# Optimization experiments

Hardware: AMD Instinct MI355X
Metric: run time of the kernel (lower is better)

The kernel has to match this reference:

```python
import jax, jax.numpy as jnp
import numpy as np

B, Z, H, W, C = 8, 16, 32, 32, 512
C8 = C // 8
N = Z * H * W
EPS = 1e-3  # Keras BatchNormalization default epsilon


def setup_inputs() -> dict:
    key = jax.random.key(0)
    ks = jax.random.split(key, 8)
    scale = 0.05
    x = jax.random.normal(ks[0], (B, Z, H, W, C), jnp.float32)
    return {
        "x": x,
        "bn1_gamma": jnp.ones((C,), jnp.float32),
        "bn1_beta": jnp.zeros((C,), jnp.float32),
        "bn1_mean": jax.random.normal(ks[1], (C,), jnp.float32) * 0.1,
        "bn1_var": jnp.abs(jax.random.normal(ks[2], (C,), jnp.float32)) * 0.1 + 1.0,
        "wq": jax.random.normal(ks[3], (C, C8), jnp.float32) * scale,
        "bq": jnp.zeros((C8,), jnp.float32),
        "wk": jax.random.normal(ks[4], (C, C8), jnp.float32) * scale,
        "bk": jnp.zeros((C8,), jnp.float32),
        "wv": jax.random.normal(ks[5], (C, C8), jnp.float32) * scale,
        "bv": jnp.zeros((C8,), jnp.float32),
        "wp": jax.random.normal(ks[6], (C8, C), jnp.float32) * scale,
        "bp": jnp.zeros((C,), jnp.float32),
        "bn2_gamma": jnp.ones((C,), jnp.float32),
        "bn2_beta": jnp.zeros((C,), jnp.float32),
        "bn2_mean": jax.random.normal(ks[7], (C,), jnp.float32) * 0.1,
        "bn2_var": jnp.ones((C,), jnp.float32),
    }


def _bn(t, gamma, beta, mean, var):
    # Keras BatchNormalization (inference), channels-last axis=-1
    return (t - mean) * jax.lax.rsqrt(var + EPS) * gamma + beta


def _conv1x1(t, w, b):
    # 1x1x1 Conv3D == per-voxel channel matmul
    return jnp.einsum('bzhwc,cd->bzhwd', t, w) + b


def reference(x, bn1_gamma, bn1_beta, bn1_mean, bn1_var,
              wq, bq, wk, bk, wv, bv, wp, bp,
              bn2_gamma, bn2_beta, bn2_mean, bn2_var):
    img = _bn(x, bn1_gamma, bn1_beta, bn1_mean, bn1_var)
    q = _conv1x1(img, wq, bq).reshape(B, N, C8)  # (B, N, c)
    k = _conv1x1(img, wk, bk).reshape(B, N, C8)  # (B, N, c)
    v = _conv1x1(img, wv, bv).reshape(B, N, C8)  # (B, N, c)
    # Keras Dot(axes=[1,2])([q, permute(k)]): contracts the N axis of both
    # -> channel Gram matrix s[b,i,j] = sum_n q[b,n,i] * k[b,n,j]
    s = jnp.einsum('bni,bnj->bij', q, k)          # (B, c, c)
    beta = jax.nn.softmax(s, axis=-1)             # (B, c, c)
    # Keras Dot(axes=[1,2])([beta, v]): attn[b,i,j] = sum_m beta[b,m,i] * v[b,j,m]
    attn = jnp.einsum('bmi,bjm->bij', beta, v)    # (B, c, N)
    # Keras Reshape((Z,H,W,c)) on (B, c, N): row-major reinterpretation
    out = attn.reshape(B, Z, H, W, C8)
    out = _conv1x1(out, wp, bp)                   # (B, Z, H, W, C)
    out = _bn(out, bn2_gamma, bn2_beta, bn2_mean, bn2_var)
    return out
```

## Files before the change

kernel.cpp:

```cpp
#include <hip/hip_runtime.h>

#define EPS 1e-3f

typedef _Float16 f16;
typedef _Float16 f16x8 __attribute__((ext_vector_type(8)));
typedef _Float16 f16x4 __attribute__((ext_vector_type(4)));
typedef float f32x4 __attribute__((ext_vector_type(4)));

constexpr int Bn = 8, C = 512, C8 = 64;
constexpr int N = 16384;
constexpr int M = Bn * N;

constexpr size_t OFF_WHI  = 0;
constexpr size_t OFF_WLO  = 196608;
constexpr size_t OFF_BQKV = 327680;
constexpr size_t OFF_WPT  = 328704;
constexpr size_t OFF_BOUT = 394240;
constexpr size_t OFF_QK   = 396288;
constexpr size_t OFF_V    = OFF_QK + (size_t)M * 128 * 2;
constexpr size_t OFF_S    = OFF_V + (size_t)M * 64 * 2;
constexpr size_t OFF_BT   = OFF_S + (size_t)8 * 4096 * 4;

__global__ __launch_bounds__(256) void k0_fold(
    const float* g1, const float* be1, const float* mu1, const float* va1,
    const float* wq, const float* bq, const float* wk, const float* bk,
    const float* wv, const float* bv, const float* wp, const float* bp,
    const float* g2, const float* be2, const float* mu2, const float* va2,
    char* ws)
{
  f16* whi = (f16*)(ws + OFF_WHI);
  f16* wlo = (f16*)(ws + OFF_WLO);
  float* bqkv = (float*)(ws + OFF_BQKV);
  f16* wpt = (f16*)(ws + OFF_WPT);
  float* bout = (float*)(ws + OFF_BOUT);
  float* sbuf = (float*)(ws + OFF_S);
  __shared__ float red[256];
  int blk = blockIdx.x, t = threadIdx.x;
  if (blk < 192) {
    const float* w; const float* bb; int col;
    if (blk < 64)       { w = wq; bb = bq; col = blk; }
    else if (blk < 128) { w = wk; bb = bk; col = blk - 64; }
    else                { w = wv; bb = bv; col = blk - 128; }
    float part = 0.f;
    for (int c = t; c < 512; c += 256) {
      float a1 = g1[c] * rsqrtf(va1[c] + EPS);
      float d1 = be1[c] - mu1[c] * a1;
      float wval = w[c * 64 + col];
      float fw = a1 * wval;
      f16 hi = (f16)fw;
      whi[blk * 512 + c] = hi;
      if (blk < 128) wlo[blk * 512 + c] = (f16)((fw - (float)hi) * 2048.0f);
      part += d1 * wval;
    }
    red[t] = part; __syncthreads();
    for (int s = 128; s > 0; s >>= 1) { if (t < s) red[t] += red[t + s]; __syncthreads(); }
    if (t == 0) bqkv[blk] = red[0] + bb[col];
  } else {
    int co = blk - 192;
    float a2 = g2[co] * rsqrtf(va2[co] + EPS);
    if (t < 64) wpt[co * 64 + t] = (f16)(wp[t * 512 + co] * a2);
    if (t == 0) bout[co] = (bp[co] - mu2[co]) * a2 + be2[co];
    if (t < 64) sbuf[co * 64 + t] = 0.0f;
  }
}

__global__ __launch_bounds__(256, 2) void k1_qkv(const float* __restrict__ x, char* __restrict__ ws)
{
  const f16* whi = (const f16*)(ws + OFF_WHI);
  const f16* wlo = (const f16*)(ws + OFF_WLO);
  const float* bqkv = (const float*)(ws + OFF_BQKV);
  f16* qkbuf = (f16*)(ws + OFF_QK);
  f16* vbuf  = (f16*)(ws + OFF_V);

  __shared__ f16 xs[2][64 * 72];

  int t = threadIdx.x;
  int wave = t >> 6, lane = t & 63;
  int m0 = blockIdx.x * 64;

  int srow = t >> 2, scol = (t & 3) * 4;
  const float* xg = x + (size_t)(m0 + srow) * 512 + scol;

  int bn0 = wave * 16 + (lane & 15);
  int bn1 = bn0 + 64;
  int bn2 = bn0 + 128;
  int klane = (lane >> 4) * 8;

  f32x4 acc_h[4][2], acc_l[4][2], acc_v[4];
  for (int i = 0; i < 4; i++) {
    for (int j = 0; j < 2; j++) { acc_h[i][j] = (f32x4){0.f,0.f,0.f,0.f}; acc_l[i][j] = (f32x4){0.f,0.f,0.f,0.f}; }
    acc_v[i] = (f32x4){0.f,0.f,0.f,0.f};
  }

  f32x4 a0 = *(const f32x4*)(xg);
  f32x4 a1 = *(const f32x4*)(xg + 16);
  f32x4 a2 = *(const f32x4*)(xg + 32);
  f32x4 a3 = *(const f32x4*)(xg + 48);

  for (int iter = 0; iter < 8; iter++) {
    f16* xb = &xs[iter & 1][0];
    {
      f16x4 h0, h1, h2, h3;
      for (int e = 0; e < 4; e++) { h0[e]=(f16)a0[e]; h1[e]=(f16)a1[e]; h2[e]=(f16)a2[e]; h3[e]=(f16)a3[e]; }
      *(f16x4*)&xb[srow * 72 + scol     ] = h0;
      *(f16x4*)&xb[srow * 72 + scol + 16] = h1;
      *(f16x4*)&xb[srow * 72 + scol + 32] = h2;
      *(f16x4*)&xb[srow * 72 + scol + 48] = h3;
    }
    __syncthreads();
    if (iter < 7) {
      const float* xi = xg + (iter + 1) * 64;
      a0 = *(const f32x4*)(xi);
      a1 = *(const f32x4*)(xi + 16);
      a2 = *(const f32x4*)(xi + 32);
      a3 = *(const f32x4*)(xi + 48);
    }
    for (int ks = 0; ks < 2; ks++) {
      int kg = iter * 64 + ks * 32 + klane;
      f16x8 b0h = *(const f16x8*)(whi + bn0 * 512 + kg);
      f16x8 b1h = *(const f16x8*)(whi + bn1 * 512 + kg);
      f16x8 b2h = *(const f16x8*)(whi + bn2 * 512 + kg);
      f16x8 b0l = *(const f16x8*)(wlo + bn0 * 512 + kg);
      f16x8 b1l = *(const f16x8*)(wlo + bn1 * 512 + kg);
      int aoff = (lane & 15) * 72 + ks * 32 + klane;
      for (int mt = 0; mt < 4; mt++) {
        f16x8 af = *(const f16x8*)&xb[mt * 16 * 72 + aoff];
        acc_h[mt][0] = __builtin_amdgcn_mfma_f32_16x16x32_f16(af, b0h, acc_h[mt][0], 0, 0, 0);
        acc_h[mt][1] = __builtin_amdgcn_mfma_f32_16x16x32_f16(af, b1h, acc_h[mt][1], 0, 0, 0);
        acc_l[mt][0] = __builtin_amdgcn_mfma_f32_16x16x32_f16(af, b0l, acc_l[mt][0], 0, 0, 0);
        acc_l[mt][1] = __builtin_amdgcn_mfma_f32_16x16x32_f16(af, b1l, acc_l[mt][1], 0, 0, 0);
        acc_v[mt]    = __builtin_amdgcn_mfma_f32_16x16x32_f16(af, b2h, acc_v[mt],    0, 0, 0);
      }
    }
  }

  const float inv2048 = 1.0f / 2048.0f;
  int colA = bn0, colB = bn1, colV = bn0;
  float bA = bqkv[colA], bB = bqkv[colB], bV = bqkv[bn2];
  int rbase = m0 + (lane >> 4) * 4;
  for (int mt = 0; mt < 4; mt++) {
    for (int r = 0; r < 4; r++) {
      size_t row = (size_t)(rbase + mt * 16 + r);
      qkbuf[row * 128 + colA] = (f16)(acc_h[mt][0][r] + acc_l[mt][0][r] * inv2048 + bA);
      qkbuf[row * 128 + colB] = (f16)(acc_h[mt][1][r] + acc_l[mt][1][r] * inv2048 + bB);
      vbuf[row * 64 + colV]   = (f16)(acc_v[mt][r] + bV);
    }
  }
}

__global__ __launch_bounds__(256) void k2a_gram(char* __restrict__ ws)
{
  const f16* qk = (const f16*)(ws + OFF_QK);
  float* sbuf = (float*)(ws + OFF_S);
  int t = threadIdx.x, wave = t >> 6, lane = t & 63;
  int b = blockIdx.x >> 6, ch = blockIdx.x & 63;
  int n0 = b * 16384 + ch * 256;

  f32x4 acc[4];
  for (int i = 0; i < 4; i++) acc[i] = (f32x4){0.f,0.f,0.f,0.f};

  int li = lane & 15;
  int jc = 64 + wave * 16 + li;

  for (int it = 0; it < 8; it++) {
    const f16* p = qk + (size_t)(n0 + it * 32 + (lane >> 4) * 8) * 128;
    f16x8 af0, af1, af2, af3, bf;
#pragma unroll
    for (int j = 0; j < 8; j++) {
      const f16* pr = p + j * 128;
      af0[j] = pr[li];
      af1[j] = pr[16 + li];
      af2[j] = pr[32 + li];
      af3[j] = pr[48 + li];
      bf[j]  = pr[jc];
    }
    acc[0] = __builtin_amdgcn_mfma_f32_16x16x32_f16(af0, bf, acc[0], 0, 0, 0);
    acc[1] = __builtin_amdgcn_mfma_f32_16x16x32_f16(af1, bf, acc[1], 0, 0, 0);
    acc[2] = __builtin_amdgcn_mfma_f32_16x16x32_f16(af2, bf, acc[2], 0, 0, 0);
    acc[3] = __builtin_amdgcn_mfma_f32_16x16x32_f16(af3, bf, acc[3], 0, 0, 0);
  }
  int j = wave * 16 + li;
  for (int itile = 0; itile < 4; itile++)
    for (int r = 0; r < 4; r++) {
      int i = itile * 16 + (lane >> 4) * 4 + r;
      atomicAdd(&sbuf[(size_t)b * 4096 + i * 64 + j], acc[itile][r]);
    }
}

__global__ __launch_bounds__(256) void k2b_softmax(char* __restrict__ ws)
{
  const float* sbuf = (const float*)(ws + OFF_S);
  f16* bt = (f16*)(ws + OFF_BT);
  int b = blockIdx.x, t = threadIdx.x;
  if (t < 64) {
    const float* srow = sbuf + (size_t)b * 4096 + t * 64;
    float mx = -1e30f;
    for (int j = 0; j < 64; j++) mx = fmaxf(mx, srow[j]);
    float e[64]; float den = 0.f;
    for (int j = 0; j < 64; j++) { e[j] = __expf(srow[j] - mx); den += e[j]; }
    float inv = 1.0f / den;
    for (int j = 0; j < 64; j++) bt[(size_t)b * 4096 + j * 64 + t] = (f16)(e[j] * inv);
  }
}

__device__ __forceinline__ int at_idx(int row, int d) {
  int dd = (d >> 1) ^ (((row >> 3) & 3) << 3);
  return row * 64 + dd * 2 + (d & 1);
}

__global__ __launch_bounds__(256, 2) void k34_attn_proj(char* __restrict__ ws, float* __restrict__ out)
{
  const f16* vbuf = (const f16*)(ws + OFF_V);
  const f16* bt = (const f16*)(ws + OFF_BT);
  const f16* wpt = (const f16*)(ws + OFF_WPT);
  const float* bout = (const float*)(ws + OFF_BOUT);
  __shared__ f16 at[128 * 64];

  int t = threadIdx.x, wave = t >> 6, lane = t & 63;
  int b = blockIdx.x >> 7, jc = blockIdx.x & 127;
  int li = lane & 15;
  int klane = (lane >> 4) * 8;

  f32x4 acc[4][2];
  for (int i = 0; i < 4; i++) for (int j = 0; j < 2; j++) acc[i][j] = (f32x4){0.f,0.f,0.f,0.f};

  for (int km = 0; km < 2; km++) {
    f16x8 af[4], bf[2];
    for (int it = 0; it < 4; it++)
      af[it] = *(const f16x8*)(bt + (size_t)b * 4096 + (it * 16 + li) * 64 + km * 32 + klane);
    for (int jt = 0; jt < 2; jt++) {
      int jrow = jc * 128 + wave * 32 + jt * 16 + li;
      bf[jt] = *(const f16x8*)(vbuf + (size_t)(b * 16384 + jrow) * 64 + km * 32 + klane);
    }
    for (int it = 0; it < 4; it++)
      for (int jt = 0; jt < 2; jt++)
        acc[it][jt] = __builtin_amdgcn_mfma_f32_16x16x32_f16(af[it], bf[jt], acc[it][jt], 0, 0, 0);
  }
  for (int it = 0; it < 4; it++)
    for (int jt = 0; jt < 2; jt++)
      for (int r = 0; r < 4; r++) {
        int i = it * 16 + (lane >> 4) * 4 + r;
        int d = (wave & 1) * 32 + jt * 16 + li;
        at[at_idx(i * 2 + (wave >> 1), d)] = (f16)acc[it][jt][r];
      }
  __syncthreads();

  f16x8 paf[2][2];
  for (int mt = 0; mt < 2; mt++)
    for (int km = 0; km < 2; km++) {
      int row = wave * 32 + mt * 16 + li;
      int d = km * 32 + klane;
      paf[mt][km] = *(const f16x8*)&at[row * 64 + ((((d >> 1) ^ (((row >> 3) & 3) << 3))) << 1)];
    }
  size_t obase = (size_t)b * 16384 * 512;
  for (int strip = 0; strip < 8; strip++) {
    int c0 = strip * 64;
    f16x8 pbf[2][4];
    for (int nt = 0; nt < 4; nt++)
      for (int km = 0; km < 2; km++)
        pbf[km][nt] = *(const f16x8*)(wpt + (size_t)(c0 + nt * 16 + li) * 64 + km * 32 + klane);
    f32x4 pac[2][4];
    for (int mt = 0; mt < 2; mt++) for (int nt = 0; nt < 4; nt++) pac[mt][nt] = (f32x4){0.f,0.f,0.f,0.f};
    for (int km = 0; km < 2; km++)
      for (int mt = 0; mt < 2; mt++)
        for (int nt = 0; nt < 4; nt++)
          pac[mt][nt] = __builtin_amdgcn_mfma_f32_16x16x32_f16(paf[mt][km], pbf[km][nt], pac[mt][nt], 0, 0, 0);
    for (int nt = 0; nt < 4; nt++) {
      int c = c0 + nt * 16 + li;
      float bc = bout[c];
      for (int mt = 0; mt < 2; mt++)
        for (int r = 0; r < 4; r++) {
          int rl = wave * 32 + mt * 16 + (lane >> 4) * 4 + r;
          int pos = (rl >> 1) * 256 + jc * 2 + (rl & 1);
          out[obase + (size_t)pos * 512 + c] = pac[mt][nt][r] + bc;
        }
    }
  }
}

extern "C" void kernel_launch(void* const* d_in, const int* in_sizes, int n_in,
                              void* d_out, int out_size, void* d_ws, size_t ws_size,
                              hipStream_t stream)
{
  const float* x   = (const float*)d_in[0];
  const float* g1  = (const float*)d_in[1];
  const float* be1 = (const float*)d_in[2];
  const float* mu1 = (const float*)d_in[3];
  const float* va1 = (const float*)d_in[4];
  const float* wq  = (const float*)d_in[5];
  const float* bq  = (const float*)d_in[6];
  const float* wk  = (const float*)d_in[7];
  const float* bk  = (const float*)d_in[8];
  const float* wv  = (const float*)d_in[9];
  const float* bv  = (const float*)d_in[10];
  const float* wp  = (const float*)d_in[11];
  const float* bp  = (const float*)d_in[12];
  const float* g2  = (const float*)d_in[13];
  const float* be2 = (const float*)d_in[14];
  const float* mu2 = (const float*)d_in[15];
  const float* va2 = (const float*)d_in[16];
  char* ws = (char*)d_ws;
  float* out = (float*)d_out;

  k0_fold<<<dim3(704), dim3(256), 0, stream>>>(g1, be1, mu1, va1, wq, bq, wk, bk,
                                               wv, bv, wp, bp, g2, be2, mu2, va2, ws);
  k1_qkv<<<dim3(2048), dim3(256), 0, stream>>>(x, ws);
  k2a_gram<<<dim3(512), dim3(256), 0, stream>>>(ws);
  k2b_softmax<<<dim3(8), dim3(256), 0, stream>>>(ws);
  k34_attn_proj<<<dim3(1024), dim3(256), 0, stream>>>(ws, out);
}
```

Measured before the change: 578.6 us.

## Fuse Q/K Gram computation into QKV projection kernel, drop QK buffer

The QKV projection kernel now stages its Q and K tile results transposed in shared memory and computes the partial 64x64 Gram matrix directly with MFMA. It atomically adds each partial into one of 8 striped partial buffers to reduce atomic contention. This removes the global Q/K round trip and the separate Gram kernel launch. The softmax kernel now sums the 8 partial buffers and uses all 256 threads with a shared-memory reduction. The cost is extra shared-memory traffic, a few more syncs in k1, and roughly 4M extra float atomics into the partial buffers.

```diff
diff --git a/kernel.cpp b/kernel.cpp
--- a/kernel.cpp
+++ b/kernel.cpp
@@ -16,10 +16,9 @@
 constexpr size_t OFF_BQKV = 327680;
 constexpr size_t OFF_WPT  = 328704;
 constexpr size_t OFF_BOUT = 394240;
-constexpr size_t OFF_QK   = 396288;
-constexpr size_t OFF_V    = OFF_QK + (size_t)M * 128 * 2;
+constexpr size_t OFF_V    = 396288;
 constexpr size_t OFF_S    = OFF_V + (size_t)M * 64 * 2;
-constexpr size_t OFF_BT   = OFF_S + (size_t)8 * 4096 * 4;
+constexpr size_t OFF_BT   = OFF_S + (size_t)8 * 8 * 4096 * 4;
 
 __global__ __launch_bounds__(256) void k0_fold(
     const float* g1, const float* be1, const float* mu1, const float* va1,
@@ -60,7 +59,8 @@
     float a2 = g2[co] * rsqrtf(va2[co] + EPS);
     if (t < 64) wpt[co * 64 + t] = (f16)(wp[t * 512 + co] * a2);
     if (t == 0) bout[co] = (bp[co] - mu2[co]) * a2 + be2[co];
-    if (t < 64) sbuf[co * 64 + t] = 0.0f;
+    sbuf[co * 512 + t] = 0.0f;
+    sbuf[co * 512 + 256 + t] = 0.0f;
   }
 }
 
@@ -69,8 +69,8 @@
   const f16* whi = (const f16*)(ws + OFF_WHI);
   const f16* wlo = (const f16*)(ws + OFF_WLO);
   const float* bqkv = (const float*)(ws + OFF_BQKV);
-  f16* qkbuf = (f16*)(ws + OFF_QK);
   f16* vbuf  = (f16*)(ws + OFF_V);
+  float* spart = (float*)(ws + OFF_S);
 
   __shared__ f16 xs[2][64 * 72];
 
@@ -135,72 +135,72 @@
   }
 
   const float inv2048 = 1.0f / 2048.0f;
-  int colA = bn0, colB = bn1, colV = bn0;
-  float bA = bqkv[colA], bB = bqkv[colB], bV = bqkv[bn2];
-  int rbase = m0 + (lane >> 4) * 4;
-  for (int mt = 0; mt < 4; mt++) {
+  float bA = bqkv[bn0], bB = bqkv[bn1], bV = bqkv[bn2];
+  f16* qT = &xs[0][0];
+  f16* kT = &xs[1][0];
+  __syncthreads();
+  for (int mt = 0; mt < 4; mt++)
     for (int r = 0; r < 4; r++) {
-      size_t row = (size_t)(rbase + mt * 16 + r);
-      qkbuf[row * 128 + colA] = (f16)(acc_h[mt][0][r] + acc_l[mt][0][r] * inv2048 + bA);
-      qkbuf[row * 128 + colB] = (f16)(acc_h[mt][1][r] + acc_l[mt][1][r] * inv2048 + bB);
-      vbuf[row * 64 + colV]   = (f16)(acc_v[mt][r] + bV);
-    }
-  }
-}
-
-__global__ __launch_bounds__(256) void k2a_gram(char* __restrict__ ws)
-{
-  const f16* qk = (const f16*)(ws + OFF_QK);
-  float* sbuf = (float*)(ws + OFF_S);
-  int t = threadIdx.x, wave = t >> 6, lane = t & 63;
-  int b = blockIdx.x >> 6, ch = blockIdx.x & 63;
-  int n0 = b * 16384 + ch * 256;
-
-  f32x4 acc[4];
-  for (int i = 0; i < 4; i++) acc[i] = (f32x4){0.f,0.f,0.f,0.f};
-
-  int li = lane & 15;
-  int jc = 64 + wave * 16 + li;
-
-  for (int it = 0; it < 8; it++) {
-    const f16* p = qk + (size_t)(n0 + it * 32 + (lane >> 4) * 8) * 128;
-    f16x8 af0, af1, af2, af3, bf;
-#pragma unroll
-    for (int j = 0; j < 8; j++) {
-      const f16* pr = p + j * 128;
-      af0[j] = pr[li];
-      af1[j] = pr[16 + li];
-      af2[j] = pr[32 + li];
-      af3[j] = pr[48 + li];
-      bf[j]  = pr[jc];
-    }
-    acc[0] = __builtin_amdgcn_mfma_f32_16x16x32_f16(af0, bf, acc[0], 0, 0, 0);
-    acc[1] = __builtin_amdgcn_mfma_f32_16x16x32_f16(af1, bf, acc[1], 0, 0, 0);
-    acc[2] = __builtin_amdgcn_mfma_f32_16x16x32_f16(af2, bf, acc[2], 0, 0, 0);
-    acc[3] = __builtin_amdgcn_mfma_f32_16x16x32_f16(af3, bf, acc[3], 0, 0, 0);
-  }
-  int j = wave * 16 + li;
-  for (int itile = 0; itile < 4; itile++)
+      int n = (lane >> 4) * 4 + mt * 16 + r;
+      size_t row = (size_t)(m0 + n);
+      float qv = acc_h[mt][0][r] + acc_l[mt][0][r] * inv2048 + bA;
+      float kv = acc_h[mt][1][r] + acc_l[mt][1][r] * inv2048 + bB;
+      qT[bn0 * 72 + n] = (f16)qv;
+      kT[bn0 * 72 + n] = (f16)kv;
+      vbuf[row * 64 + bn0] = (f16)(acc_v[mt][r] + bV);
+    }
+  __syncthreads();
+
+  f32x4 gacc[4];
+  for (int i = 0; i < 4; i++) gacc[i] = (f32x4){0.f,0.f,0.f,0.f};
+  for (int ks = 0; ks < 2; ks++) {
+    f16x8 bfr = *(const f16x8*)&kT[(wave * 16 + (lane & 15)) * 72 + ks * 32 + klane];
+    for (int it = 0; it < 4; it++) {
+      f16x8 afr = *(const f16x8*)&qT[(it * 16 + (lane & 15)) * 72 + ks * 32 + klane];
+      gacc[it] = __builtin_amdgcn_mfma_f32_16x16x32_f16(afr, bfr, gacc[it], 0, 0, 0);
+    }
+  }
+  int b = blockIdx.x >> 8;
+  int g = blockIdx.x & 7;
+  float* sdst = spart + ((size_t)(g * 8 + b)) * 4096;
+  int j = wave * 16 + (lane & 15);
+  for (int it = 0; it < 4; it++)
     for (int r = 0; r < 4; r++) {
-      int i = itile * 16 + (lane >> 4) * 4 + r;
-      atomicAdd(&sbuf[(size_t)b * 4096 + i * 64 + j], acc[itile][r]);
+      int i = it * 16 + (lane >> 4) * 4 + r;
+      atomicAdd(&sdst[i * 64 + j], gacc[it][r]);
     }
 }
 
 __global__ __launch_bounds__(256) void k2b_softmax(char* __restrict__ ws)
 {
-  const float* sbuf = (const float*)(ws + OFF_S);
+  const float* spart = (const float*)(ws + OFF_S);
   f16* bt = (f16*)(ws + OFF_BT);
+  __shared__ float red[64][4];
+
   int b = blockIdx.x, t = threadIdx.x;
-  if (t < 64) {
-    const float* srow = sbuf + (size_t)b * 4096 + t * 64;
-    float mx = -1e30f;
-    for (int j = 0; j < 64; j++) mx = fmaxf(mx, srow[j]);
-    float e[64]; float den = 0.f;
-    for (int j = 0; j < 64; j++) { e[j] = __expf(srow[j] - mx); den += e[j]; }
-    float inv = 1.0f / den;
-    for (int j = 0; j < 64; j++) bt[(size_t)b * 4096 + j * 64 + t] = (f16)(e[j] * inv);
-  }
+  int m = t & 63, qd = t >> 6;
+
+  float sv[16];
+  {
+    const float* base = spart + (size_t)b * 4096 + (size_t)m * 64 + qd * 16;
+    f32x4 v0 = (f32x4){0.f,0.f,0.f,0.f}, v1 = v0, v2 = v0, v3 = v0;
+    for (int g = 0; g < 8; g++) {
+      const f32x4* p = (const f32x4*)(base + (size_t)g * 8 * 4096);
+      v0 += p[0]; v1 += p[1]; v2 += p[2]; v3 += p[3];
+    }
+    for (int e = 0; e < 4; e++) { sv[e] = v0[e]; sv[4+e] = v1[e]; sv[8+e] = v2[e]; sv[12+e] = v3[e]; }
+  }
+  float mx = sv[0];
+  for (int jj = 1; jj < 16; jj++) mx = fmaxf(mx, sv[jj]);
+  red[m][qd] = mx; __syncthreads();
+  float rmx = fmaxf(fmaxf(red[m][0], red[m][1]), fmaxf(red[m][2], red[m][3]));
+  __syncthreads();
+  float s = 0.f;
+  for (int jj = 0; jj < 16; jj++) { float e = __expf(sv[jj] - rmx); sv[jj] = e; s += e; }
+  red[m][qd] = s; __syncthreads();
+  float inv = 1.0f / (red[m][0] + red[m][1] + red[m][2] + red[m][3]);
+  for (int jj = 0; jj < 16; jj++)
+    bt[(size_t)b * 4096 + (qd * 16 + jj) * 64 + m] = (f16)(sv[jj] * inv);
 }
 
 __device__ __forceinline__ int at_idx(int row, int d) {
@@ -305,7 +305,6 @@
   k0_fold<<<dim3(704), dim3(256), 0, stream>>>(g1, be1, mu1, va1, wq, bq, wk, bk,
                                                wv, bv, wp, bp, g2, be2, mu2, va2, ws);
   k1_qkv<<<dim3(2048), dim3(256), 0, stream>>>(x, ws);
-  k2a_gram<<<dim3(512), dim3(256), 0, stream>>>(ws);
   k2b_softmax<<<dim3(8), dim3(256), 0, stream>>>(ws);
   k34_attn_proj<<<dim3(1024), dim3(256), 0, stream>>>(ws, out);
 }
```

After: 571.2 us. No clear change (-1.3%).
